# Optimization experiments

Measured on AMD Instinct MI355X. Metric: run time of the kernel, lower is better.

The kernel has to match this reference:

```python
import jax, jax.numpy as jnp
import numpy as np

M, N, D = 131072, 4000, 16

def setup_inputs() -> dict:
    key = jax.random.key(0)
    k1, k2, k3 = jax.random.split(key, 3)
    cse_embedding = jax.random.normal(k1, (M, D), dtype=jnp.float32)
    verts_colors = jax.random.uniform(k2, (N, 3), dtype=jnp.float32)
    verts_cse_embedding = jax.random.normal(k3, (N, D), dtype=jnp.float32)
    return {
        "cse_embedding": cse_embedding,
        "verts_colors": verts_colors,
        "verts_cse_embedding": verts_cse_embedding,
    }

def reference(cse_embedding, verts_colors, verts_cse_embedding):
    # Nearest neighbor in Euclidean distance == argmin of squared distance.
    # scores: (M, N)
    y_sq = jnp.sum(verts_cse_embedding * verts_cse_embedding, axis=-1)  # (N,)
    scores = y_sq[None, :] - 2.0 * jnp.einsum('md,nd->mn', cse_embedding, verts_cse_embedding)
    closest_verts = jnp.argmin(scores, axis=-1)  # (M,) int
    rendered_colors = verts_colors[closest_verts]  # (M, 3) gather
    return rendered_colors
```

## Files before the change

### kernel.cpp

```cpp
#include <hip/hip_runtime.h>
#include <math.h>
#include <stdint.h>

#define M_ROWS   131072
#define N_VERTS  4000
#define N_PAD    4096
#define D_DIM    16
#define N_TILES  (N_PAD / 32)
#define TILE_B   3072
#define CHUNK_T  8
#define CHUNK_B  (CHUNK_T * TILE_B)
#define N_CHUNKS (N_TILES / CHUNK_T)

#define SCORE_BIAS 128.0f
#define TIE_EPS 0.03f

#define WS_YFRAG_OFF 0
#define WS_CNT_OFF   393216
#define WS_LIST_OFF  393280

typedef float f32x16 __attribute__((ext_vector_type(16)));
typedef short s16x8  __attribute__((ext_vector_type(8)));

__device__ __forceinline__ unsigned short f32_to_bf16_rne(float f) {
    unsigned int u = __float_as_uint(f);
    u = (u + 0x7fffu + ((u >> 16) & 1u)) >> 16;
    return (unsigned short)u;
}
__device__ __forceinline__ float bf16_to_f32(unsigned short h) {
    return __uint_as_float(((unsigned int)h) << 16);
}
__device__ __forceinline__ uint32_t umin32(uint32_t a, uint32_t b) { return a < b ? a : b; }
__device__ __forceinline__ uint32_t umax32(uint32_t a, uint32_t b) { return a > b ? a : b; }

__device__ __forceinline__ uint32_t med3_u32(uint32_t a, uint32_t b, uint32_t c) {
    uint32_t d;
    asm("v_med3_u32 %0, %1, %2, %3" : "=v"(d) : "v"(a), "v"(b), "v"(c));
    return d;
}

__global__ void pack_y_kernel(const float* __restrict__ verts,
                              char* __restrict__ yfrag,
                              int* __restrict__ cnt) {
    const int tid = blockIdx.x * blockDim.x + threadIdx.x;
    if (tid == 0) *cnt = 0;

    const int T   = tid >> 6;
    const int l   = tid & 63;
    const int col = l & 31;
    const int h   = l >> 5;
    const int n   = T * 32 + col;
    const int d0  = h * 8;

    float v[8];
    if (n < N_VERTS) {
        const float* y = verts + (size_t)n * D_DIM + d0;
#pragma unroll
        for (int j = 0; j < 8; ++j) v[j] = y[j];
    } else {
#pragma unroll
        for (int j = 0; j < 8; ++j) v[j] = 0.f;
    }
    s16x8 fh, fl;
#pragma unroll
    for (int j = 0; j < 8; ++j) {
        const unsigned short hh = f32_to_bf16_rne(v[j]);
        fh[j] = (short)hh;
        fl[j] = (short)f32_to_bf16_rne(v[j] - bf16_to_f32(hh));
    }
    char* tb = yfrag + (size_t)T * TILE_B + (size_t)l * 16;
    *(s16x8*)(tb)        = fh;
    *(s16x8*)(tb + 1024) = fl;

    s16x8 fy;
#pragma unroll
    for (int j = 0; j < 8; ++j) fy[j] = 0;
    if (h == 0) {
        float ys;
        if (n < N_VERTS) {
            ys = SCORE_BIAS;
            const float* y = verts + (size_t)n * D_DIM;
#pragma unroll
            for (int d = 0; d < D_DIM; ++d) ys = fmaf(y[d], y[d], ys);
        } else {
            ys = 1e30f;
        }
        const unsigned short ysh = f32_to_bf16_rne(ys);
        fy[0] = (short)ysh;
        fy[1] = (short)f32_to_bf16_rne(ys - bf16_to_f32(ysh));
    }
    *(s16x8*)(tb + 2048) = fy;
}

__global__ __launch_bounds__(512, 4) void mfma_screen_kernel(
    const float* __restrict__ x_all,
    const float* __restrict__ colors,
    const char* __restrict__ yfrag,
    float* __restrict__ out,
    int* __restrict__ cnt,
    int* __restrict__ list,
    int list_cap)
{
    __shared__ __align__(16) char s_buf[2 * CHUNK_B];

    const int tid  = threadIdx.x;
    const int wave = tid >> 6;
    const int lane = tid & 63;
    const int col  = lane & 31;
    const int h    = lane >> 5;
    const int rowBase = blockIdx.x * 256 + wave * 32;

    const float* xr = x_all + (size_t)(rowBase + col) * D_DIM + h * 8;
    const float4 xa = *(const float4*)xr;
    const float4 xb = *(const float4*)(xr + 4);
    const float xv[8] = {xa.x, xa.y, xa.z, xa.w, xb.x, xb.y, xb.z, xb.w};
    s16x8 a1, a2;
#pragma unroll
    for (int j = 0; j < 8; ++j) {
        const float a = -2.0f * xv[j];
        const unsigned short hh = f32_to_bf16_rne(a);
        a1[j] = (short)hh;
        a2[j] = (short)f32_to_bf16_rne(a - bf16_to_f32(hh));
    }
    s16x8 aone;
#pragma unroll
    for (int j = 0; j < 8; ++j) aone[j] = 0;
    if (h == 0) { aone[0] = (short)0x3F80; aone[1] = (short)0x3F80; }

    f32x16 zero16;
#pragma unroll
    for (int r = 0; r < 16; ++r) zero16[r] = 0.f;

    const int4* gy = (const int4*)yfrag;
    int4 ra = gy[tid];
    int4 rb = gy[512 + tid];
    int4 rc = gy[1024 + tid];
    {
        int4* s = (int4*)s_buf;
        s[tid] = ra; s[512 + tid] = rb; s[1024 + tid] = rc;
    }

    uint32_t best[16], second[16];
#pragma unroll
    for (int r = 0; r < 16; ++r) { best[r] = 0xFFFFFFFFu; second[r] = 0xFFFFFFFFu; }

    for (int ch = 0; ch < N_CHUNKS; ++ch) {
        if (ch + 1 < N_CHUNKS) {
            const int base = (ch + 1) * 1536;
            ra = gy[base + tid];
            rb = gy[base + 512 + tid];
            rc = gy[base + 1024 + tid];
        }
        __syncthreads();

        const char* bb = s_buf + (ch & 1) * CHUNK_B + lane * 16;
#pragma unroll 1
        for (int t = 0; t < CHUNK_T; ++t) {
            const s16x8 byh = *(const s16x8*)(bb + t * TILE_B);
            const s16x8 byl = *(const s16x8*)(bb + t * TILE_B + 1024);
            const s16x8 bys = *(const s16x8*)(bb + t * TILE_B + 2048);
            f32x16 acc = __builtin_amdgcn_mfma_f32_32x32x16_bf16(a1, byh, zero16, 0, 0, 0);
            acc = __builtin_amdgcn_mfma_f32_32x32x16_bf16(a2, byh, acc, 0, 0, 0);
            acc = __builtin_amdgcn_mfma_f32_32x32x16_bf16(a1, byl, acc, 0, 0, 0);
            acc = __builtin_amdgcn_mfma_f32_32x32x16_bf16(aone, bys, acc, 0, 0, 0);
            const uint32_t tcur = (uint32_t)(ch * CHUNK_T + t);
#pragma unroll
            for (int r = 0; r < 16; ++r) {
                const uint32_t kb = (__float_as_uint(acc[r]) & 0xFFFFFF00u) | tcur;
                second[r] = med3_u32(best[r], kb, second[r]);
                best[r]   = umin32(best[r], kb);
            }
        }
        if (ch + 1 < N_CHUNKS) {
            int4* s = (int4*)(s_buf + ((ch + 1) & 1) * CHUNK_B);
            s[tid] = ra; s[512 + tid] = rb; s[1024 + tid] = rc;
        }
    }

    __syncthreads();
    uint32_t* s_red = (uint32_t*)s_buf;
#pragma unroll
    for (int r = 0; r < 16; ++r) {
        const int row = (r & 3) + 8 * (r >> 2) + 4 * h;
        s_red[wave * 1024 + row * 32 + col] = best[r];
    }
    __syncthreads();

    uint32_t b1 = 0xFFFFFFFFu, b2 = 0xFFFFFFFFu;
    int cwin = 0;
    if (tid < 256) {
        const int w = tid >> 5, row = tid & 31;
#pragma unroll
        for (int c = 0; c < 32; ++c) {
            const uint32_t k = s_red[w * 1024 + row * 32 + c];
            cwin = (k < b1) ? c : cwin;
            b2 = umin32(b2, umax32(b1, k));
            b1 = umin32(b1, k);
        }
    }
    __syncthreads();
#pragma unroll
    for (int r = 0; r < 16; ++r) {
        const int row = (r & 3) + 8 * (r >> 2) + 4 * h;
        s_red[wave * 1024 + row * 32 + col] = second[r];
    }
    __syncthreads();

    if (tid < 256) {
        const int w = tid >> 5, row = tid & 31;
        uint32_t smin = 0xFFFFFFFFu;
#pragma unroll
        for (int c = 0; c < 32; ++c)
            smin = umin32(smin, s_red[w * 1024 + row * 32 + c]);
        const uint32_t secondAll = umin32(smin, b2);
        const float s1 = __uint_as_float(b1 & 0xFFFFFF00u);
        const float s2 = __uint_as_float(secondAll & 0xFFFFFF00u);
        const int n = (int)(b1 & 0xFFu) * 32 + cwin;
        const int m = blockIdx.x * 256 + tid;

        bool amb = (s2 - s1 <= TIE_EPS);
        if (amb) {
            const int pos = atomicAdd(cnt, 1);
            if (pos < list_cap) list[pos] = m;
            else amb = false;
        }
        if (!amb) {
            const float* cc2 = colors + (size_t)n * 3;
            float* o = out + (size_t)m * 3;
            o[0] = cc2[0];
            o[1] = cc2[1];
            o[2] = cc2[2];
        }
    }
}

__global__ __launch_bounds__(256) void rescan_kernel(
    const float* __restrict__ x_all,
    const float* __restrict__ colors,
    const float* __restrict__ verts,
    const int* __restrict__ cnt,
    const int* __restrict__ list,
    int list_cap,
    float* __restrict__ out)
{
    const int wavesPerBlock = blockDim.x >> 6;
    const int wid  = blockIdx.x * wavesPerBlock + (threadIdx.x >> 6);
    const int lane = threadIdx.x & 63;
    const int nWaves = gridDim.x * wavesPerBlock;

    int ccount = *cnt;
    if (ccount > list_cap) ccount = list_cap;

    for (int rr = wid; rr < ccount; rr += nWaves) {
        const int m = list[rr];
        double bx[D_DIM];
#pragma unroll
        for (int d = 0; d < D_DIM; ++d)
            bx[d] = (double)x_all[(size_t)m * D_DIM + d];

        double best = INFINITY;
        int bi = 0x7fffffff;
#pragma unroll 2
        for (int n = lane; n < N_VERTS; n += 64) {
            const float* y = verts + (size_t)n * D_DIM;
            double dot = 0.0, ys = 0.0;
#pragma unroll
            for (int d = 0; d < D_DIM; ++d) {
                const double yd = (double)y[d];
                dot = fma(bx[d], yd, dot);
                ys  = fma(yd, yd, ys);
            }
            const double s = ys - 2.0 * dot;
            if (s < best || (s == best && n < bi)) { best = s; bi = n; }
        }
#pragma unroll
        for (int off = 32; off > 0; off >>= 1) {
            const double ob = __shfl_xor(best, off, 64);
            const int    oi = __shfl_xor(bi, off, 64);
            if (ob < best || (ob == best && oi < bi)) { best = ob; bi = oi; }
        }
        if (lane == 0) {
            const float* cc = colors + (size_t)bi * 3;
            float* o = out + (size_t)m * 3;
            o[0] = cc[0];
            o[1] = cc[1];
            o[2] = cc[2];
        }
    }
}

extern "C" void kernel_launch(void* const* d_in, const int* in_sizes, int n_in,
                              void* d_out, int out_size, void* d_ws, size_t ws_size,
                              hipStream_t stream) {
    const float* cse_embedding       = (const float*)d_in[0];
    const float* verts_colors        = (const float*)d_in[1];
    const float* verts_cse_embedding = (const float*)d_in[2];
    float* out = (float*)d_out;

    char* ws = (char*)d_ws;
    char*  yfrag = ws + WS_YFRAG_OFF;
    int*   cnt   = (int*)(ws + WS_CNT_OFF);
    int*   list  = (int*)(ws + WS_LIST_OFF);
    int list_cap = (int)((ws_size > WS_LIST_OFF)
                         ? ((ws_size - WS_LIST_OFF) / sizeof(int)) : 0);
    if (list_cap > M_ROWS) list_cap = M_ROWS;

    pack_y_kernel<<<(N_TILES * 64) / 256, 256, 0, stream>>>(
        verts_cse_embedding, yfrag, cnt);

    mfma_screen_kernel<<<M_ROWS / 256, 512, 0, stream>>>(
        cse_embedding, verts_colors, yfrag, out, cnt, list, list_cap);

    rescan_kernel<<<2048, 256, 0, stream>>>(
        cse_embedding, verts_colors, verts_cse_embedding, cnt, list,
        list_cap, out);
}
```

Baseline: 198.3 us.

## Split vertex range across two blocks per row tile and merge partial argmins

The screen kernel now splits the 4096 padded vertices into halves, launching twice as many blocks. Each block writes its best key, second-best key and winning index to workspace partial buffers. A new merge kernel combines the two halves, applies the tie-ambiguity test and either writes the color or queues the row for rescan. Chunk size is halved and launch bounds raised to lower LDS and register use for higher occupancy. The cost is an extra kernel launch and extra global traffic for the partial results.

```diff
diff --git a/kernel.cpp b/kernel.cpp
--- a/kernel.cpp
+++ b/kernel.cpp
@@ -8,16 +8,14 @@
 #define D_DIM    16
 #define N_TILES  (N_PAD / 32)
 #define TILE_B   3072
-#define CHUNK_T  8
+#define CHUNK_T  4
 #define CHUNK_B  (CHUNK_T * TILE_B)
-#define N_CHUNKS (N_TILES / CHUNK_T)
 
 #define SCORE_BIAS 128.0f
 #define TIE_EPS 0.03f
 
 #define WS_YFRAG_OFF 0
-#define WS_CNT_OFF   393216
-#define WS_LIST_OFF  393280
+#define WS_PART_OFF  393216
 
 typedef float f32x16 __attribute__((ext_vector_type(16)));
 typedef short s16x8  __attribute__((ext_vector_type(8)));
@@ -92,23 +90,28 @@
     *(s16x8*)(tb + 2048) = fy;
 }
 
-__global__ __launch_bounds__(512, 4) void mfma_screen_kernel(
+__global__ __launch_bounds__(512, 8) void mfma_screen_kernel(
     const float* __restrict__ x_all,
-    const float* __restrict__ colors,
     const char* __restrict__ yfrag,
-    float* __restrict__ out,
-    int* __restrict__ cnt,
-    int* __restrict__ list,
-    int list_cap)
+    uint32_t* __restrict__ pbk,
+    uint32_t* __restrict__ psk,
+    uint32_t* __restrict__ pn,
+    int lsplit)
 {
-    __shared__ __align__(16) char s_buf[2 * CHUNK_B];
-
+    __shared__ __align__(16) char s_buf[32768];
+
+    const int bid  = blockIdx.x;
+    const int half = bid & ((1 << lsplit) - 1);
+    const int mb   = bid >> lsplit;
     const int tid  = threadIdx.x;
     const int wave = tid >> 6;
     const int lane = tid & 63;
     const int col  = lane & 31;
     const int h    = lane >> 5;
-    const int rowBase = blockIdx.x * 256 + wave * 32;
+    const int rowBase = mb * 256 + wave * 32;
+
+    const int tileBase = half * (N_TILES >> lsplit);
+    const int nchunks  = (N_TILES >> lsplit) / CHUNK_T;
 
     const float* xr = x_all + (size_t)(rowBase + col) * D_DIM + h * 8;
     const float4 xa = *(const float4*)xr;
@@ -131,12 +134,12 @@
 #pragma unroll
     for (int r = 0; r < 16; ++r) zero16[r] = 0.f;
 
-    const int4* gy = (const int4*)yfrag;
-    int4 ra = gy[tid];
-    int4 rb = gy[512 + tid];
-    int4 rc = gy[1024 + tid];
+    const int2* gy = (const int2*)(yfrag + (size_t)tileBase * TILE_B);
+    int2 ra = gy[tid];
+    int2 rb = gy[512 + tid];
+    int2 rc = gy[1024 + tid];
     {
-        int4* s = (int4*)s_buf;
+        int2* s = (int2*)s_buf;
         s[tid] = ra; s[512 + tid] = rb; s[1024 + tid] = rc;
     }
 
@@ -144,8 +147,8 @@
 #pragma unroll
     for (int r = 0; r < 16; ++r) { best[r] = 0xFFFFFFFFu; second[r] = 0xFFFFFFFFu; }
 
-    for (int ch = 0; ch < N_CHUNKS; ++ch) {
-        if (ch + 1 < N_CHUNKS) {
+    for (int ch = 0; ch < nchunks; ++ch) {
+        if (ch + 1 < nchunks) {
             const int base = (ch + 1) * 1536;
             ra = gy[base + tid];
             rb = gy[base + 512 + tid];
@@ -163,7 +166,7 @@
             acc = __builtin_amdgcn_mfma_f32_32x32x16_bf16(a2, byh, acc, 0, 0, 0);
             acc = __builtin_amdgcn_mfma_f32_32x32x16_bf16(a1, byl, acc, 0, 0, 0);
             acc = __builtin_amdgcn_mfma_f32_32x32x16_bf16(aone, bys, acc, 0, 0, 0);
-            const uint32_t tcur = (uint32_t)(ch * CHUNK_T + t);
+            const uint32_t tcur = (uint32_t)(tileBase + ch * CHUNK_T + t);
 #pragma unroll
             for (int r = 0; r < 16; ++r) {
                 const uint32_t kb = (__float_as_uint(acc[r]) & 0xFFFFFF00u) | tcur;
@@ -171,8 +174,8 @@
                 best[r]   = umin32(best[r], kb);
             }
         }
-        if (ch + 1 < N_CHUNKS) {
-            int4* s = (int4*)(s_buf + ((ch + 1) & 1) * CHUNK_B);
+        if (ch + 1 < nchunks) {
+            int2* s = (int2*)(s_buf + ((ch + 1) & 1) * CHUNK_B);
             s[tid] = ra; s[512 + tid] = rb; s[1024 + tid] = rc;
         }
     }
@@ -207,30 +210,59 @@
     __syncthreads();
 
     if (tid < 256) {
+        uint32_t smin = 0xFFFFFFFFu;
         const int w = tid >> 5, row = tid & 31;
-        uint32_t smin = 0xFFFFFFFFu;
 #pragma unroll
         for (int c = 0; c < 32; ++c)
             smin = umin32(smin, s_red[w * 1024 + row * 32 + c]);
-        const uint32_t secondAll = umin32(smin, b2);
-        const float s1 = __uint_as_float(b1 & 0xFFFFFF00u);
-        const float s2 = __uint_as_float(secondAll & 0xFFFFFF00u);
-        const int n = (int)(b1 & 0xFFu) * 32 + cwin;
-        const int m = blockIdx.x * 256 + tid;
-
-        bool amb = (s2 - s1 <= TIE_EPS);
-        if (amb) {
-            const int pos = atomicAdd(cnt, 1);
-            if (pos < list_cap) list[pos] = m;
-            else amb = false;
-        }
-        if (!amb) {
-            const float* cc2 = colors + (size_t)n * 3;
-            float* o = out + (size_t)m * 3;
-            o[0] = cc2[0];
-            o[1] = cc2[1];
-            o[2] = cc2[2];
-        }
+        const int m = mb * 256 + tid;
+        const size_t idx = (size_t)half * M_ROWS + m;
+        pbk[idx] = b1;
+        psk[idx] = umin32(smin, b2);
+        pn[idx]  = (b1 & 0xFFu) * 32 + (uint32_t)cwin;
+    }
+}
+
+__global__ __launch_bounds__(256) void merge_kernel(
+    const uint32_t* __restrict__ pbk,
+    const uint32_t* __restrict__ psk,
+    const uint32_t* __restrict__ pn,
+    const float* __restrict__ colors,
+    float* __restrict__ out,
+    int* __restrict__ cnt,
+    int* __restrict__ list,
+    int list_cap,
+    int nsplit)
+{
+    const int m = blockIdx.x * 256 + threadIdx.x;
+    if (m >= M_ROWS) return;
+
+    uint32_t b = pbk[m];
+    uint32_t s = psk[m];
+    uint32_t n = pn[m];
+    if (nsplit == 2) {
+        const uint32_t b1 = pbk[M_ROWS + m];
+        const uint32_t s1 = psk[M_ROWS + m];
+        const uint32_t n1 = pn[M_ROWS + m];
+        s = umin32(umin32(s, s1), umax32(b, b1));
+        if (b1 < b) n = n1;
+        b = umin32(b, b1);
+    }
+    const float sc1 = __uint_as_float(b & 0xFFFFFF00u);
+    const float sc2 = __uint_as_float(s & 0xFFFFFF00u);
+
+    bool amb = (sc2 - sc1 <= TIE_EPS);
+    if (amb) {
+        const int pos = atomicAdd(cnt, 1);
+        if (pos < list_cap) list[pos] = m;
+        else amb = false;
+    }
+    if (!amb) {
+        const float* cc = colors + (size_t)n * 3;
+        float* o = out + (size_t)m * 3;
+        o[0] = cc[0];
+        o[1] = cc[1];
+        o[2] = cc[2];
     }
 }
 
@@ -298,18 +330,32 @@
     float* out = (float*)d_out;
 
     char* ws = (char*)d_ws;
-    char*  yfrag = ws + WS_YFRAG_OFF;
-    int*   cnt   = (int*)(ws + WS_CNT_OFF);
-    int*   list  = (int*)(ws + WS_LIST_OFF);
-    int list_cap = (int)((ws_size > WS_LIST_OFF)
-                         ? ((ws_size - WS_LIST_OFF) / sizeof(int)) : 0);
+    char* yfrag = ws + WS_YFRAG_OFF;
+
+    const size_t partB = (size_t)M_ROWS * 4;
+    size_t need2 = WS_PART_OFF + 6 * partB + 64 + 64 * 1024;
+    int nsplit = (ws_size >= need2) ? 2 : 1;
+    const int lsplit = (nsplit == 2) ? 1 : 0;
+
+    uint32_t* pbk = (uint32_t*)(ws + WS_PART_OFF);
+    uint32_t* psk = (uint32_t*)(ws + WS_PART_OFF + (size_t)nsplit * partB);
+    uint32_t* pn  = (uint32_t*)(ws + WS_PART_OFF + 2 * (size_t)nsplit * partB);
+    size_t cntOff = WS_PART_OFF + 3 * (size_t)nsplit * partB;
+    cntOff = (cntOff + 63) & ~(size_t)63;
+    int* cnt  = (int*)(ws + cntOff);
+    int* list = (int*)(ws + cntOff + 64);
+    int list_cap = (ws_size > cntOff + 64)
+                   ? (int)((ws_size - cntOff - 64) / sizeof(int)) : 0;
     if (list_cap > M_ROWS) list_cap = M_ROWS;
 
     pack_y_kernel<<<(N_TILES * 64) / 256, 256, 0, stream>>>(
         verts_cse_embedding, yfrag, cnt);
 
-    mfma_screen_kernel<<<M_ROWS / 256, 512, 0, stream>>>(
-        cse_embedding, verts_colors, yfrag, out, cnt, list, list_cap);
+    mfma_screen_kernel<<<(M_ROWS / 256) * nsplit, 512, 0, stream>>>(
+        cse_embedding, yfrag, pbk, psk, pn, lsplit);
+
+    merge_kernel<<<M_ROWS / 256, 256, 0, stream>>>(
+        pbk, psk, pn, verts_colors, out, cnt, list, list_cap, nsplit);
 
     rescan_kernel<<<2048, 256, 0, stream>>>(
         cse_embedding, verts_colors, verts_cse_embedding, cnt, list,
```

Result: slower. 363.0 us (+83.0%).
